# Optimization experiments

Hardware: AMD Instinct MI355X
Metric: run time of the kernel (lower is better)

Reference implementation:

```python
import jax, jax.numpy as jnp
import numpy as np

N_NODES = 50000
N_EDGES = 800000
NUM_GRAPHS = 4
IN_DIM, HID_DIM, OUT_DIM = 1024, 128, 1
MAX_RISK = 5.0


def gcn_conv(x, W, b, src, dst, n):
    """PyG GCNConv: add self-loops, sym-normalize, gather-GEMM-scatter."""
    loop = jnp.arange(n, dtype=src.dtype)
    s = jnp.concatenate([src, loop])
    d = jnp.concatenate([dst, loop])
    deg = jax.ops.segment_sum(jnp.ones_like(d, dtype=x.dtype), d, num_segments=n)
    dinv = jnp.where(deg > 0, jax.lax.rsqrt(deg), 0.0)
    norm = dinv[s] * dinv[d]  # [E+N]
    xw = x @ W                # dense GEMM first (fewer FLOPs than per-edge)
    msg = xw[s] * norm[:, None]          # irregular gather, [E+N, out]
    out = jax.ops.segment_sum(msg, d, num_segments=n)  # scatter-add
    return out + b


def setup_inputs() -> dict:
    key = jax.random.key(0)
    ks = jax.random.split(key, 12)
    x = jax.random.normal(ks[0], (N_NODES, IN_DIM), dtype=jnp.float32)
    edge_index = jax.random.randint(ks[1], (2, N_EDGES), 0, N_NODES, dtype=jnp.int64)
    batch = jnp.sort(jax.random.randint(ks[2], (N_NODES,), 0, NUM_GRAPHS, dtype=jnp.int64))

    def glorot(k, fan_in, fan_out):
        s = np.sqrt(6.0 / (fan_in + fan_out)).astype(np.float32)
        return jax.random.uniform(k, (fan_in, fan_out), jnp.float32, -s, s)

    params = {
        'W0': glorot(ks[3], IN_DIM, HID_DIM),  'b0': jnp.zeros((HID_DIM,), jnp.float32),
        'W1': glorot(ks[4], HID_DIM, HID_DIM), 'b1': jnp.zeros((HID_DIM,), jnp.float32),
        'W2': glorot(ks[5], HID_DIM, HID_DIM), 'b2': jnp.zeros((HID_DIM,), jnp.float32),
        'Wl1': glorot(ks[6], 2 * HID_DIM, HID_DIM), 'bl1': jnp.zeros((HID_DIM,), jnp.float32),
        'Wl2': glorot(ks[7], HID_DIM, HID_DIM // 2), 'bl2': jnp.zeros((HID_DIM // 2,), jnp.float32),
        'Wl3': glorot(ks[8], HID_DIM // 2, OUT_DIM), 'bl3': jnp.zeros((OUT_DIM,), jnp.float32),
    }
    return dict(x=x, edge_index=edge_index, batch=batch, **params)


def reference(x, edge_index, batch, W0, b0, W1, b1, W2, b2, Wl1, bl1, Wl2, bl2, Wl3, bl3):
    n = x.shape[0]
    src, dst = edge_index[0], edge_index[1]
    h = jax.nn.relu(gcn_conv(x, W0, b0, src, dst, n))
    h = jax.nn.relu(gcn_conv(h, W1, b1, src, dst, n))
    h = jax.nn.relu(gcn_conv(h, W2, b2, src, dst, n))
    # global max pool + global mean pool per graph
    gmax = jax.ops.segment_max(h, batch, num_segments=NUM_GRAPHS)
    gsum = jax.ops.segment_sum(h, batch, num_segments=NUM_GRAPHS)
    cnt = jax.ops.segment_sum(jnp.ones((n,), h.dtype), batch, num_segments=NUM_GRAPHS)
    gmean = gsum / jnp.maximum(cnt, 1.0)[:, None]
    g = jnp.concatenate([gmax, gmean], axis=1)  # [G, 2*hid]
    g = jax.nn.relu(g @ Wl1 + bl1)
    g = jax.nn.relu(g @ Wl2 + bl2)
    out = g @ Wl3 + bl3
    return jnp.minimum(out, MAX_RISK)
```

## Files before the change

### kernel.cpp

```cpp
#include <hip/hip_runtime.h>
#include <math.h>

#define HID 128
#define NGRAPH 4

typedef int idx_t;
typedef float f32x4 __attribute__((ext_vector_type(4)));
typedef _Float16 h8 __attribute__((ext_vector_type(8)));

__device__ inline int sw(int row, int slot) {
  return (row << 5) + ((slot ^ ((row >> 1) & 3)) << 3);
}

__global__ __launch_bounds__(256) void k_count(const idx_t* __restrict__ dst,
                                               int* __restrict__ cnt, int E) {
  int e = blockIdx.x * 256 + threadIdx.x;
  if (e < E) atomicAdd(&cnt[dst[e]], 1);
}

#define SC 1024
__global__ __launch_bounds__(256) void k_scan1(const int* __restrict__ cnt,
                                               int* __restrict__ bsum, int n) {
  __shared__ int sh[256];
  int base = blockIdx.x * SC + threadIdx.x * 4;
  int s = 0;
#pragma unroll
  for (int j = 0; j < 4; ++j) { int i = base + j; if (i < n) s += cnt[i]; }
  sh[threadIdx.x] = s;
  __syncthreads();
  for (int o = 128; o > 0; o >>= 1) {
    if (threadIdx.x < o) sh[threadIdx.x] += sh[threadIdx.x + o];
    __syncthreads();
  }
  if (threadIdx.x == 0) bsum[blockIdx.x] = sh[0];
}

__global__ __launch_bounds__(64) void k_scan2(const int* __restrict__ bsum,
                                              int* __restrict__ boff,
                                              int* __restrict__ off, int nb, int n) {
  int lane = threadIdx.x;
  int v = (lane < nb) ? bsum[lane] : 0;
  for (int d = 1; d < 64; d <<= 1) {
    int t = __shfl_up(v, d);
    if (lane >= d) v += t;
  }
  int ex = __shfl_up(v, 1);
  if (lane == 0) ex = 0;
  if (lane < nb) boff[lane] = ex;
  if (lane == nb - 1) off[n] = v;
}

__global__ __launch_bounds__(256) void k_scan3(const int* __restrict__ cnt,
                                               const int* __restrict__ boff,
                                               int* __restrict__ off,
                                               float* __restrict__ dinv, int n) {
  __shared__ int sh[256];
  int base = blockIdx.x * SC + threadIdx.x * 4;
  int c[4];
  int s = 0;
#pragma unroll
  for (int j = 0; j < 4; ++j) {
    int i = base + j;
    c[j] = (i < n) ? cnt[i] : 0;
    s += c[j];
  }
  sh[threadIdx.x] = s;
  __syncthreads();
  for (int o = 1; o < 256; o <<= 1) {
    int t = (threadIdx.x >= (unsigned)o) ? sh[threadIdx.x - o] : 0;
    __syncthreads();
    sh[threadIdx.x] += t;
    __syncthreads();
  }
  int ex = sh[threadIdx.x] - s + boff[blockIdx.x];
#pragma unroll
  for (int j = 0; j < 4; ++j) {
    int i = base + j;
    if (i < n) {
      off[i] = ex;
      dinv[i] = 1.0f / sqrtf((float)c[j] + 1.0f);
      ex += c[j];
    }
  }
}

__global__ __launch_bounds__(256) void k_fill(const idx_t* __restrict__ src,
                                              const idx_t* __restrict__ dst,
                                              const int* __restrict__ off,
                                              const float* __restrict__ dinv,
                                              int* __restrict__ fillc,
                                              int2* __restrict__ edata, int E) {
  int e = blockIdx.x * 256 + threadIdx.x;
  if (e < E) {
    int s = src[e], d = dst[e];
    int p = atomicAdd(&fillc[d], 1);
    float w = dinv[s] * dinv[d];
    edata[off[d] + p] = make_int2(s, __float_as_int(w));
  }
}

__global__ __launch_bounds__(256) void k_wsplit(const float* __restrict__ W,
                                                _Float16* __restrict__ Wh,
                                                _Float16* __restrict__ Wl, int K) {
  int i = blockIdx.x * 256 + threadIdx.x;
  if (i >= K * HID) return;
  int k = i >> 7, n = i & 127;
  float f = W[i];
  _Float16 h = (_Float16)f;
  Wh[(size_t)n * K + k] = h;
  Wl[(size_t)n * K + k] = (_Float16)(f - (float)h);
}

template <int K, bool F32>
__global__ __launch_bounds__(256) void k_gemm3(const void* __restrict__ Xv,
                                               const _Float16* __restrict__ Wh,
                                               const _Float16* __restrict__ Wl,
                                               _Float16* __restrict__ Y16, int M) {
  __shared__ __align__(16) _Float16 BhL[2][128 * 32];
  __shared__ __align__(16) _Float16 BlL[2][128 * 32];
  const int tid = threadIdx.x;
  const int wid = tid >> 6, lane = tid & 63;
  const int lrow = lane & 15, kg = lane >> 4;
  const int row0 = blockIdx.x * 64;
  const int r = row0 + wid * 16 + lrow;
  const int rc = (r < M) ? r : 0;
  const float* xf = (const float*)Xv + (size_t)rc * K + kg * 8;
  const _Float16* xg = (const _Float16*)Xv + (size_t)rc * K + kg * 8;
  const int c0 = tid >> 2, s0 = tid & 3;
  const int c1 = 64 + c0;
  const _Float16* wh0 = Wh + (size_t)c0 * K + s0 * 8;
  const _Float16* wh1 = Wh + (size_t)c1 * K + s0 * 8;
  const _Float16* wl0 = Wl + (size_t)c0 * K + s0 * 8;
  const _Float16* wl1 = Wl + (size_t)c1 * K + s0 * 8;
  const int d0 = sw(c0, s0), d1 = sw(c1, s0);

  f32x4 acc[8] = {};
  float4 aA0, aA1, aB0, aB1;
  h8 gA, gB;
  h8 bA0, bA1, bA2, bA3, bB0, bB1, bB2, bB3;

#define LOAD_A0(k0)                                                       \
  { if (F32) { aA0 = *(const float4*)(xf + (k0));                         \
               aA1 = *(const float4*)(xf + (k0) + 4); }                   \
    else gA = *(const h8*)(xg + (k0)); }
#define LOAD_A1(k0)                                                       \
  { if (F32) { aB0 = *(const float4*)(xf + (k0));                         \
               aB1 = *(const float4*)(xf + (k0) + 4); }                   \
    else gB = *(const h8*)(xg + (k0)); }
#define LOAD_B(k0, b0, b1, b2, b3)                                        \
  { b0 = *(const h8*)(wh0 + (k0)); b1 = *(const h8*)(wh1 + (k0));         \
    b2 = *(const h8*)(wl0 + (k0)); b3 = *(const h8*)(wl1 + (k0)); }
#define WRITE_B(buf, b0, b1, b2, b3)                                      \
  { *(h8*)&BhL[buf][d0] = b0; *(h8*)&BhL[buf][d1] = b1;                   \
    *(h8*)&BlL[buf][d0] = b2; *(h8*)&BlL[buf][d1] = b3; }
#define CONV(v0, v1, g, ah, al)                                           \
  { if (F32) {                                                            \
      float tf[8] = {v0.x, v0.y, v0.z, v0.w, v1.x, v1.y, v1.z, v1.w};     \
      _Pragma("unroll")                                                   \
      for (int j = 0; j < 8; ++j) {                                       \
        _Float16 hh = (_Float16)tf[j];                                    \
        ah[j] = hh; al[j] = (_Float16)(tf[j] - (float)hh);                \
      }                                                                   \
    } else ah = g; }
#define MFMA_STEP(buf, ah, al)                                            \
  { _Pragma("unroll")                                                     \
    for (int ni = 0; ni < 8; ++ni) {                                      \
      int c = ni * 16 + lrow;                                             \
      h8 bh = *(const h8*)&BhL[buf][sw(c, kg)];                           \
      h8 bl = *(const h8*)&BlL[buf][sw(c, kg)];                           \
      acc[ni] = __builtin_amdgcn_mfma_f32_16x16x32_f16(ah, bh, acc[ni], 0, 0, 0); \
      if (F32)                                                            \
        acc[ni] = __builtin_amdgcn_mfma_f32_16x16x32_f16(al, bh, acc[ni], 0, 0, 0); \
      acc[ni] = __builtin_amdgcn_mfma_f32_16x16x32_f16(ah, bl, acc[ni], 0, 0, 0); \
    } }

  LOAD_A0(0);
  LOAD_B(0, bA0, bA1, bA2, bA3);
  WRITE_B(0, bA0, bA1, bA2, bA3);
  if (K > 32) {
    LOAD_A1(32);
    LOAD_B(32, bB0, bB1, bB2, bB3);
  }
  __syncthreads();

  for (int k0 = 0; k0 < K; k0 += 64) {
    {
      if (k0 + 32 < K) WRITE_B(1, bB0, bB1, bB2, bB3);
      h8 ah, al;
      CONV(aA0, aA1, gA, ah, al);
      if (k0 + 64 < K) {
        LOAD_A0(k0 + 64);
        LOAD_B(k0 + 64, bA0, bA1, bA2, bA3);
      }
      MFMA_STEP(0, ah, al);
      __syncthreads();
    }
    if (k0 + 32 >= K) break;
    {
      if (k0 + 96 < K) WRITE_B(0, bA0, bA1, bA2, bA3);
      h8 ah, al;
      CONV(aB0, aB1, gB, ah, al);
      if (k0 + 96 < K) {
        LOAD_A1(k0 + 96);
        LOAD_B(k0 + 96, bB0, bB1, bB2, bB3);
      }
      MFMA_STEP(1, ah, al);
      __syncthreads();
    }
  }
#pragma unroll
  for (int ni = 0; ni < 8; ++ni)
#pragma unroll
    for (int rr = 0; rr < 4; ++rr) {
      int grow = row0 + wid * 16 + kg * 4 + rr;
      if (grow < M)
        Y16[(size_t)grow * HID + ni * 16 + lrow] = (_Float16)acc[ni][rr];
    }
#undef LOAD_A0
#undef LOAD_A1
#undef LOAD_B
#undef WRITE_B
#undef CONV
#undef MFMA_STEP
}

__global__ __launch_bounds__(256) void k_agg16(const _Float16* __restrict__ xh,
                                               const float* __restrict__ dinv,
                                               const int* __restrict__ off,
                                               const int2* __restrict__ edata,
                                               const float* __restrict__ bias,
                                               _Float16* __restrict__ hout, int n) {
  int v = blockIdx.x * 4 + (threadIdx.x >> 6);
  if (v >= n) return;
  int lane = threadIdx.x & 63;
  int grp = lane >> 3, gl = lane & 7;
  int fb = gl * 16;
  float acc[16] = {0.f, 0.f, 0.f, 0.f, 0.f, 0.f, 0.f, 0.f,
                   0.f, 0.f, 0.f, 0.f, 0.f, 0.f, 0.f, 0.f};
  int j0 = off[v], j1 = off[v + 1];
  for (int j = j0 + grp; j < j1; j += 8) {
    int2 e = edata[j];
    float w = __int_as_float(e.y);
    h8 m0 = *(const h8*)&xh[(size_t)e.x * HID + fb];
    h8 m1 = *(const h8*)&xh[(size_t)e.x * HID + fb + 8];
#pragma unroll
    for (int q = 0; q < 8; ++q) {
      acc[q] = fmaf(w, (float)m0[q], acc[q]);
      acc[8 + q] = fmaf(w, (float)m1[q], acc[8 + q]);
    }
  }
#pragma unroll
  for (int q = 0; q < 16; ++q) {
    acc[q] += __shfl_xor(acc[q], 8);
    acc[q] += __shfl_xor(acc[q], 16);
    acc[q] += __shfl_xor(acc[q], 32);
  }
  if (grp == 0) {
    float dv = dinv[v], dv2 = dv * dv;
    h8 s0 = *(const h8*)&xh[(size_t)v * HID + fb];
    h8 s1 = *(const h8*)&xh[(size_t)v * HID + fb + 8];
    h8 o0, o1;
#pragma unroll
    for (int q = 0; q < 8; ++q) {
      float a0 = fmaxf(fmaf(dv2, (float)s0[q], acc[q]) + bias[fb + q], 0.f);
      float a1 = fmaxf(fmaf(dv2, (float)s1[q], acc[8 + q]) + bias[fb + 8 + q], 0.f);
      o0[q] = (_Float16)a0;
      o1[q] = (_Float16)a1;
    }
    *(h8*)&hout[(size_t)v * HID + fb] = o0;
    *(h8*)&hout[(size_t)v * HID + fb + 8] = o1;
  }
}

__global__ __launch_bounds__(256) void k_gcnt(const idx_t* __restrict__ batch,
                                              int* __restrict__ gcnt, int n) {
  __shared__ int h[NGRAPH];
  int tid = threadIdx.x;
  if (tid < NGRAPH) h[tid] = 0;
  __syncthreads();
  int i = blockIdx.x * 256 + tid;
  if (i < n) atomicAdd(&h[batch[i]], 1);
  __syncthreads();
  if (tid < NGRAPH && h[tid]) atomicAdd(&gcnt[tid], h[tid]);
}

__global__ __launch_bounds__(128) void k_pool(const _Float16* __restrict__ h,
                                              const idx_t* __restrict__ batch,
                                              float* __restrict__ gmax,
                                              float* __restrict__ gsum, int n) {
  int f = threadIdx.x;
  int v0 = blockIdx.x * 128;
  int cur = -1;
  float mx = 0.f, sm = 0.f;
  for (int i = 0; i < 128; ++i) {
    int v = v0 + i;
    if (v >= n) break;
    int g = batch[v];
    if (g != cur) {
      if (cur >= 0) {
        atomicMax((int*)&gmax[cur * HID + f], __float_as_int(mx));
        atomicAdd(&gsum[cur * HID + f], sm);
      }
      cur = g; mx = 0.f; sm = 0.f;
    }
    float val = (float)h[(size_t)v * HID + f];
    mx = fmaxf(mx, val);
    sm += val;
  }
  if (cur >= 0) {
    atomicMax((int*)&gmax[cur * HID + f], __float_as_int(mx));
    atomicAdd(&gsum[cur * HID + f], sm);
  }
}

__global__ __launch_bounds__(256) void k_mlp(const float* __restrict__ gmax,
                                             const float* __restrict__ gsum,
                                             const int* __restrict__ gcnt,
                                             const float* __restrict__ Wl1,
                                             const float* __restrict__ bl1,
                                             const float* __restrict__ Wl2,
                                             const float* __restrict__ bl2,
                                             const float* __restrict__ Wl3,
                                             const float* __restrict__ bl3,
                                             float* __restrict__ out) {
  __shared__ float G[NGRAPH][2 * HID];
  __shared__ float H1[NGRAPH][HID];
  __shared__ float H2[NGRAPH][HID / 2];
  int t = threadIdx.x;
  for (int i = t; i < NGRAPH * 2 * HID; i += 256) {
    int gi = i >> 8, j = i & 255;
    float val;
    if (j < HID) val = gmax[gi * HID + j];
    else val = gsum[gi * HID + (j - HID)] / fmaxf((float)gcnt[gi], 1.0f);
    G[gi][j] = val;
  }
  __syncthreads();
  for (int i = t; i < NGRAPH * HID; i += 256) {
    int gi = i >> 7, j = i & 127;
    float a = bl1[j];
    for (int k = 0; k < 2 * HID; ++k) a = fmaf(G[gi][k], Wl1[k * HID + j], a);
    H1[gi][j] = fmaxf(a, 0.f);
  }
  __syncthreads();
  {
    int gi = t >> 6, j = t & 63;
    float a = bl2[j];
    for (int k = 0; k < HID; ++k) a = fmaf(H1[gi][k], Wl2[k * 64 + j], a);
    H2[gi][j] = fmaxf(a, 0.f);
  }
  __syncthreads();
  if (t < NGRAPH) {
    float a = bl3[0];
    for (int k = 0; k < 64; ++k) a = fmaf(H2[t][k], Wl3[k], a);
    out[t] = fminf(a, 5.0f);
  }
}

extern "C" void kernel_launch(void* const* d_in, const int* in_sizes, int n_in,
                              void* d_out, int out_size, void* d_ws, size_t ws_size,
                              hipStream_t stream) {
  const float* x   = (const float*)d_in[0];
  const idx_t* ei  = (const idx_t*)d_in[1];
  const idx_t* bat = (const idx_t*)d_in[2];
  const float* W0 = (const float*)d_in[3];  const float* b0 = (const float*)d_in[4];
  const float* W1 = (const float*)d_in[5];  const float* b1 = (const float*)d_in[6];
  const float* W2 = (const float*)d_in[7];  const float* b2 = (const float*)d_in[8];
  const float* Wl1 = (const float*)d_in[9];  const float* bl1 = (const float*)d_in[10];
  const float* Wl2 = (const float*)d_in[11]; const float* bl2 = (const float*)d_in[12];
  const float* Wl3 = (const float*)d_in[13]; const float* bl3 = (const float*)d_in[14];
  float* out = (float*)d_out;

  const int N = in_sizes[2];
  const int E = in_sizes[1] / 2;
  const idx_t* srcv = ei;
  const idx_t* dstv = ei + E;
  const int nb = (N + SC - 1) / SC;

  char* ws = (char*)d_ws;
  size_t o = 0;
  auto alloc = [&](size_t bytes) -> void* {
    void* p = ws + o;
    o = (o + bytes + 255) & ~(size_t)255;
    return p;
  };
  _Float16* xh  = (_Float16*)alloc((size_t)N * HID * 2);
  _Float16* h16 = (_Float16*)alloc((size_t)N * HID * 2);
  float* dinv = (float*)alloc((size_t)N * 4);
  int* cnt    = (int*)alloc((size_t)N * 4);
  int* off    = (int*)alloc((size_t)(N + 1) * 4);
  int* fillc  = (int*)alloc((size_t)N * 4);
  int2* edata = (int2*)alloc((size_t)E * 8);
  int* bsum   = (int*)alloc(64 * 4);
  int* boff   = (int*)alloc(64 * 4);
  _Float16* Wh0 = (_Float16*)alloc((size_t)1024 * HID * 2);
  _Float16* Wl0 = (_Float16*)alloc((size_t)1024 * HID * 2);
  _Float16* Wh1 = (_Float16*)alloc((size_t)HID * HID * 2);
  _Float16* Wlo1 = (_Float16*)alloc((size_t)HID * HID * 2);
  _Float16* Wh2 = (_Float16*)alloc((size_t)HID * HID * 2);
  _Float16* Wlo2 = (_Float16*)alloc((size_t)HID * HID * 2);
  float* gmax = (float*)alloc(NGRAPH * HID * 4);
  float* gsum = (float*)alloc(NGRAPH * HID * 4);
  int* gcnt   = (int*)alloc(NGRAPH * 4);

  hipMemsetAsync(cnt, 0, (size_t)N * 4, stream);
  hipMemsetAsync(fillc, 0, (size_t)N * 4, stream);
  hipMemsetAsync(gmax, 0, NGRAPH * HID * 4, stream);
  hipMemsetAsync(gsum, 0, NGRAPH * HID * 4, stream);
  hipMemsetAsync(gcnt, 0, NGRAPH * 4, stream);

  k_wsplit<<<(1024 * HID + 255) / 256, 256, 0, stream>>>(W0, Wh0, Wl0, 1024);
  k_wsplit<<<(HID * HID + 255) / 256, 256, 0, stream>>>(W1, Wh1, Wlo1, HID);
  k_wsplit<<<(HID * HID + 255) / 256, 256, 0, stream>>>(W2, Wh2, Wlo2, HID);

  k_count<<<(E + 255) / 256, 256, 0, stream>>>(dstv, cnt, E);
  k_scan1<<<nb, 256, 0, stream>>>(cnt, bsum, N);
  k_scan2<<<1, 64, 0, stream>>>(bsum, boff, off, nb, N);
  k_scan3<<<nb, 256, 0, stream>>>(cnt, boff, off, dinv, N);
  k_fill<<<(E + 255) / 256, 256, 0, stream>>>(srcv, dstv, off, dinv, fillc, edata, E);

  const int gblk = (N + 63) / 64;
  const int ablk = (N + 3) / 4;
  k_gemm3<1024, true><<<gblk, 256, 0, stream>>>(x, Wh0, Wl0, xh, N);
  k_agg16<<<ablk, 256, 0, stream>>>(xh, dinv, off, edata, b0, h16, N);
  k_gemm3<HID, false><<<gblk, 256, 0, stream>>>(h16, Wh1, Wlo1, xh, N);
  k_agg16<<<ablk, 256, 0, stream>>>(xh, dinv, off, edata, b1, h16, N);
  k_gemm3<HID, false><<<gblk, 256, 0, stream>>>(h16, Wh2, Wlo2, xh, N);
  k_agg16<<<ablk, 256, 0, stream>>>(xh, dinv, off, edata, b2, h16, N);

  k_gcnt<<<(N + 255) / 256, 256, 0, stream>>>(bat, gcnt, N);
  k_pool<<<(N + 127) / 128, 128, 0, stream>>>(h16, bat, gmax, gsum, N);
  k_mlp<<<1, 256, 0, stream>>>(gmax, gsum, gcnt, Wl1, bl1, Wl2, bl2, Wl3, bl3, out);
}
```

Before: 370.6 us.

## Replace LDS-staged GEMM with single-wave kernel reading weights from global

Rewrites the node-feature GEMM as a one-wavefront block that computes a 32x128 tile. B fragments come straight from global memory (L2/L1) instead of being staged through double-buffered shared memory, which removes the LDS writes and block barriers. Each loaded weight fragment is reused across two 16-row A tiles. The cost is more global and cache traffic for weights per row and less latency hiding, since there is no explicit prefetch.

```diff
diff --git a/kernel.cpp b/kernel.cpp
--- a/kernel.cpp
+++ b/kernel.cpp
@@ -7,10 +7,6 @@
 typedef int idx_t;
 typedef float f32x4 __attribute__((ext_vector_type(4)));
 typedef _Float16 h8 __attribute__((ext_vector_type(8)));
-
-__device__ inline int sw(int row, int slot) {
-  return (row << 5) + ((slot ^ ((row >> 1) & 3)) << 3);
-}
 
 __global__ __launch_bounds__(256) void k_count(const idx_t* __restrict__ dst,
                                                int* __restrict__ cnt, int E) {
@@ -112,116 +108,67 @@
 }
 
 template <int K, bool F32>
-__global__ __launch_bounds__(256) void k_gemm3(const void* __restrict__ Xv,
-                                               const _Float16* __restrict__ Wh,
-                                               const _Float16* __restrict__ Wl,
-                                               _Float16* __restrict__ Y16, int M) {
-  __shared__ __align__(16) _Float16 BhL[2][128 * 32];
-  __shared__ __align__(16) _Float16 BlL[2][128 * 32];
-  const int tid = threadIdx.x;
-  const int wid = tid >> 6, lane = tid & 63;
+__global__ __launch_bounds__(64) void k_gemm4(const void* __restrict__ Xv,
+                                              const _Float16* __restrict__ Wh,
+                                              const _Float16* __restrict__ Wl,
+                                              _Float16* __restrict__ Y16, int M) {
+  const int lane = threadIdx.x & 63;
   const int lrow = lane & 15, kg = lane >> 4;
-  const int row0 = blockIdx.x * 64;
-  const int r = row0 + wid * 16 + lrow;
-  const int rc = (r < M) ? r : 0;
-  const float* xf = (const float*)Xv + (size_t)rc * K + kg * 8;
-  const _Float16* xg = (const _Float16*)Xv + (size_t)rc * K + kg * 8;
-  const int c0 = tid >> 2, s0 = tid & 3;
-  const int c1 = 64 + c0;
-  const _Float16* wh0 = Wh + (size_t)c0 * K + s0 * 8;
-  const _Float16* wh1 = Wh + (size_t)c1 * K + s0 * 8;
-  const _Float16* wl0 = Wl + (size_t)c0 * K + s0 * 8;
-  const _Float16* wl1 = Wl + (size_t)c1 * K + s0 * 8;
-  const int d0 = sw(c0, s0), d1 = sw(c1, s0);
-
-  f32x4 acc[8] = {};
-  float4 aA0, aA1, aB0, aB1;
-  h8 gA, gB;
-  h8 bA0, bA1, bA2, bA3, bB0, bB1, bB2, bB3;
-
-#define LOAD_A0(k0)                                                       \
-  { if (F32) { aA0 = *(const float4*)(xf + (k0));                         \
-               aA1 = *(const float4*)(xf + (k0) + 4); }                   \
-    else gA = *(const h8*)(xg + (k0)); }
-#define LOAD_A1(k0)                                                       \
-  { if (F32) { aB0 = *(const float4*)(xf + (k0));                         \
-               aB1 = *(const float4*)(xf + (k0) + 4); }                   \
-    else gB = *(const h8*)(xg + (k0)); }
-#define LOAD_B(k0, b0, b1, b2, b3)                                        \
-  { b0 = *(const h8*)(wh0 + (k0)); b1 = *(const h8*)(wh1 + (k0));         \
-    b2 = *(const h8*)(wl0 + (k0)); b3 = *(const h8*)(wl1 + (k0)); }
-#define WRITE_B(buf, b0, b1, b2, b3)                                      \
-  { *(h8*)&BhL[buf][d0] = b0; *(h8*)&BhL[buf][d1] = b1;                   \
-    *(h8*)&BlL[buf][d0] = b2; *(h8*)&BlL[buf][d1] = b3; }
-#define CONV(v0, v1, g, ah, al)                                           \
-  { if (F32) {                                                            \
-      float tf[8] = {v0.x, v0.y, v0.z, v0.w, v1.x, v1.y, v1.z, v1.w};     \
-      _Pragma("unroll")                                                   \
-      for (int j = 0; j < 8; ++j) {                                       \
-        _Float16 hh = (_Float16)tf[j];                                    \
-        ah[j] = hh; al[j] = (_Float16)(tf[j] - (float)hh);                \
-      }                                                                   \
-    } else ah = g; }
-#define MFMA_STEP(buf, ah, al)                                            \
-  { _Pragma("unroll")                                                     \
-    for (int ni = 0; ni < 8; ++ni) {                                      \
-      int c = ni * 16 + lrow;                                             \
-      h8 bh = *(const h8*)&BhL[buf][sw(c, kg)];                           \
-      h8 bl = *(const h8*)&BlL[buf][sw(c, kg)];                           \
-      acc[ni] = __builtin_amdgcn_mfma_f32_16x16x32_f16(ah, bh, acc[ni], 0, 0, 0); \
-      if (F32)                                                            \
-        acc[ni] = __builtin_amdgcn_mfma_f32_16x16x32_f16(al, bh, acc[ni], 0, 0, 0); \
-      acc[ni] = __builtin_amdgcn_mfma_f32_16x16x32_f16(ah, bl, acc[ni], 0, 0, 0); \
-    } }
-
-  LOAD_A0(0);
-  LOAD_B(0, bA0, bA1, bA2, bA3);
-  WRITE_B(0, bA0, bA1, bA2, bA3);
-  if (K > 32) {
-    LOAD_A1(32);
-    LOAD_B(32, bB0, bB1, bB2, bB3);
-  }
-  __syncthreads();
-
-  for (int k0 = 0; k0 < K; k0 += 64) {
-    {
-      if (k0 + 32 < K) WRITE_B(1, bB0, bB1, bB2, bB3);
-      h8 ah, al;
-      CONV(aA0, aA1, gA, ah, al);
-      if (k0 + 64 < K) {
-        LOAD_A0(k0 + 64);
-        LOAD_B(k0 + 64, bA0, bA1, bA2, bA3);
+  const int row0 = blockIdx.x * 32;
+  const int ra = row0 + lrow, rb = row0 + 16 + lrow;
+  const int rca = (ra < M) ? ra : 0, rcb = (rb < M) ? rb : 0;
+  const float* xf0 = (const float*)Xv + (size_t)rca * K + kg * 8;
+  const float* xf1 = (const float*)Xv + (size_t)rcb * K + kg * 8;
+  const _Float16* xg0 = (const _Float16*)Xv + (size_t)rca * K + kg * 8;
+  const _Float16* xg1 = (const _Float16*)Xv + (size_t)rcb * K + kg * 8;
+  const _Float16* bh_p = Wh + (size_t)lrow * K + kg * 8;
+  const _Float16* bl_p = Wl + (size_t)lrow * K + kg * 8;
+
+  f32x4 acc[2][8] = {};
+
+  for (int k0 = 0; k0 < K; k0 += 32) {
+    h8 ah0, al0, ah1, al1;
+    if (F32) {
+      float4 a0 = *(const float4*)(xf0 + k0);
+      float4 a1 = *(const float4*)(xf0 + k0 + 4);
+      float4 a2 = *(const float4*)(xf1 + k0);
+      float4 a3 = *(const float4*)(xf1 + k0 + 4);
+      float t0[8] = {a0.x, a0.y, a0.z, a0.w, a1.x, a1.y, a1.z, a1.w};
+      float t1[8] = {a2.x, a2.y, a2.z, a2.w, a3.x, a3.y, a3.z, a3.w};
+#pragma unroll
+      for (int j = 0; j < 8; ++j) {
+        _Float16 h0 = (_Float16)t0[j], h1 = (_Float16)t1[j];
+        ah0[j] = h0; al0[j] = (_Float16)(t0[j] - (float)h0);
+        ah1[j] = h1; al1[j] = (_Float16)(t1[j] - (float)h1);
       }
-      MFMA_STEP(0, ah, al);
-      __syncthreads();
-    }
-    if (k0 + 32 >= K) break;
-    {
-      if (k0 + 96 < K) WRITE_B(0, bA0, bA1, bA2, bA3);
-      h8 ah, al;
-      CONV(aB0, aB1, gB, ah, al);
-      if (k0 + 96 < K) {
-        LOAD_A1(k0 + 96);
-        LOAD_B(k0 + 96, bB0, bB1, bB2, bB3);
+    } else {
+      ah0 = *(const h8*)(xg0 + k0);
+      ah1 = *(const h8*)(xg1 + k0);
+    }
+#pragma unroll
+    for (int ni = 0; ni < 8; ++ni) {
+      h8 bh = *(const h8*)(bh_p + (size_t)ni * 16 * K + k0);
+      h8 bl = *(const h8*)(bl_p + (size_t)ni * 16 * K + k0);
+      acc[0][ni] = __builtin_amdgcn_mfma_f32_16x16x32_f16(ah0, bh, acc[0][ni], 0, 0, 0);
+      acc[1][ni] = __builtin_amdgcn_mfma_f32_16x16x32_f16(ah1, bh, acc[1][ni], 0, 0, 0);
+      if (F32) {
+        acc[0][ni] = __builtin_amdgcn_mfma_f32_16x16x32_f16(al0, bh, acc[0][ni], 0, 0, 0);
+        acc[1][ni] = __builtin_amdgcn_mfma_f32_16x16x32_f16(al1, bh, acc[1][ni], 0, 0, 0);
       }
-      MFMA_STEP(1, ah, al);
-      __syncthreads();
-    }
-  }
-#pragma unroll
-  for (int ni = 0; ni < 8; ++ni)
-#pragma unroll
-    for (int rr = 0; rr < 4; ++rr) {
-      int grow = row0 + wid * 16 + kg * 4 + rr;
-      if (grow < M)
-        Y16[(size_t)grow * HID + ni * 16 + lrow] = (_Float16)acc[ni][rr];
-    }
-#undef LOAD_A0
-#undef LOAD_A1
-#undef LOAD_B
-#undef WRITE_B
-#undef CONV
-#undef MFMA_STEP
+      acc[0][ni] = __builtin_amdgcn_mfma_f32_16x16x32_f16(ah0, bl, acc[0][ni], 0, 0, 0);
+      acc[1][ni] = __builtin_amdgcn_mfma_f32_16x16x32_f16(ah1, bl, acc[1][ni], 0, 0, 0);
+    }
+  }
+#pragma unroll
+  for (int mi = 0; mi < 2; ++mi)
+#pragma unroll
+    for (int ni = 0; ni < 8; ++ni)
+#pragma unroll
+      for (int rr = 0; rr < 4; ++rr) {
+        int grow = row0 + mi * 16 + kg * 4 + rr;
+        if (grow < M)
+          Y16[(size_t)grow * HID + ni * 16 + lrow] = (_Float16)acc[mi][ni][rr];
+      }
 }
 
 __global__ __launch_bounds__(256) void k_agg16(const _Float16* __restrict__ xh,
@@ -418,13 +365,13 @@
   k_scan3<<<nb, 256, 0, stream>>>(cnt, boff, off, dinv, N);
   k_fill<<<(E + 255) / 256, 256, 0, stream>>>(srcv, dstv, off, dinv, fillc, edata, E);
 
-  const int gblk = (N + 63) / 64;
+  const int gblk = (N + 31) / 32;
   const int ablk = (N + 3) / 4;
-  k_gemm3<1024, true><<<gblk, 256, 0, stream>>>(x, Wh0, Wl0, xh, N);
+  k_gemm4<1024, true><<<gblk, 64, 0, stream>>>(x, Wh0, Wl0, xh, N);
   k_agg16<<<ablk, 256, 0, stream>>>(xh, dinv, off, edata, b0, h16, N);
-  k_gemm3<HID, false><<<gblk, 256, 0, stream>>>(h16, Wh1, Wlo1, xh, N);
+  k_gemm4<HID, false><<<gblk, 64, 0, stream>>>(h16, Wh1, Wlo1, xh, N);
   k_agg16<<<ablk, 256, 0, stream>>>(xh, dinv, off, edata, b1, h16, N);
-  k_gemm3<HID, false><<<gblk, 256, 0, stream>>>(h16, Wh2, Wlo2, xh, N);
+  k_gemm4<HID, false><<<gblk, 64, 0, stream>>>(h16, Wh2, Wlo2, xh, N);
   k_agg16<<<ablk, 256, 0, stream>>>(xh, dinv, off, edata, b2, h16, N);
 
   k_gcnt<<<(N + 255) / 256, 256, 0, stream>>>(bat, gcnt, N);
```

After: 451.7 us. +21.9%, slower.
